# Kernel tuning notes

Measured on AMD Instinct MI355X. Metric: run time of the kernel, lower is better.

The kernel has to match this reference:

```python
import jax, jax.numpy as jnp
import numpy as np

B, N, D, S = 128, 1024, 512, 64
ITERS = 3
EPS = 1e-8


def setup_inputs() -> dict:
    key = jax.random.key(0)
    ks = jax.random.split(key, 10)
    inp = {
        "inputs_pe": jax.random.normal(ks[0], (B, N, D), dtype=jnp.float32),
        "inputs": jax.random.normal(ks[1], (B, N, D), dtype=jnp.float32),
        "slots": jax.random.normal(ks[2], (1, S, D), dtype=jnp.float32),
        "W1": jax.random.normal(ks[3], (D, D), dtype=jnp.float32) * 0.02,
        "b1": jnp.zeros((D,), dtype=jnp.float32),
        "W2": jax.random.normal(ks[4], (D, D), dtype=jnp.float32) * 0.02,
        "b2": jnp.zeros((D,), dtype=jnp.float32),
        "W3": jax.random.normal(ks[5], (D, D), dtype=jnp.float32) * 0.02,
        "b3": jnp.zeros((D,), dtype=jnp.float32),
    }
    return inp


def reference(inputs_pe, inputs, slots, W1, b1, W2, b2, W3, b3):
    b = inputs_pe.shape[0]
    scale = D ** (-0.5)
    # to_k: Linear -> ReLU -> Linear -> ReLU -> Linear (torch Linear: x @ W.T + b)
    h = jax.nn.relu(jnp.einsum('bnd,ed->bne', inputs_pe, W1) + b1)
    h = jax.nn.relu(jnp.einsum('bnd,ed->bne', h, W2) + b2)
    k = jnp.einsum('bnd,ed->bne', h, W3) + b3  # [b, n, d]

    q = jnp.broadcast_to(slots, (b, S, D))  # slots never updated in the loop
    for _ in range(ITERS):
        dots = jnp.einsum('bid,bjd->bij', q, k) * scale  # [b, S, n]
        s_j = dots.sum(axis=2, keepdims=True)            # sum over keys j -> [b, S, 1]
        s_all = dots.sum(axis=(1, 2), keepdims=True)     # total per batch -> [b, 1, 1]
        dots = dots / s_j * s_all
        attn = jax.nn.sigmoid(dots)
        attn2 = attn / (attn.sum(axis=-1, keepdims=True) + EPS)
        updates = jnp.einsum('bjd,bij->bid', inputs, attn2)  # [b, S, d]
    return updates, attn
```

## Files before the change

kernel.cpp:

```cpp
#include <hip/hip_runtime.h>
#include <stdint.h>

#define Bb 128
#define Nn 1024
#define Dd 512
#define Ss 64

constexpr float kScale = 0.044194173824159216f;
constexpr float kEps = 1e-8f;

typedef __bf16 bf16x8 __attribute__((ext_vector_type(8)));
typedef float f32x4 __attribute__((ext_vector_type(4)));
typedef float f32x16 __attribute__((ext_vector_type(16)));

#define MFMA32 __builtin_amdgcn_mfma_f32_32x32x16_bf16

__device__ inline unsigned short f2bf_rne(float x) {
  unsigned u = __builtin_bit_cast(unsigned, x);
  u += 0x7FFFu + ((u >> 16) & 1u);
  return (unsigned short)(u >> 16);
}
__device__ inline float bf2f(unsigned short h) {
  unsigned u = ((unsigned)h) << 16;
  return __builtin_bit_cast(float, u);
}

__device__ inline void gl_lds16(const void* g, void* l) {
  typedef unsigned int u32;
  auto gp = (u32 __attribute__((address_space(1)))*)(unsigned long long)(uintptr_t)g;
  auto lp = (u32 __attribute__((address_space(3)))*)(unsigned int)(uintptr_t)l;
  __builtin_amdgcn_global_load_lds(gp, lp, 16, 0, 0);
}

__global__ void cast_split(const float* __restrict__ in,
                           unsigned short* __restrict__ hi,
                           unsigned short* __restrict__ lo,
                           int n4) {
  int i = blockIdx.x * blockDim.x + threadIdx.x;
  const int stride = gridDim.x * blockDim.x;
  for (; i < n4; i += stride) {
    const float4 v = ((const float4*)in)[i];
    ushort4 h, lw;
    h.x = f2bf_rne(v.x); lw.x = f2bf_rne(v.x - bf2f(h.x));
    h.y = f2bf_rne(v.y); lw.y = f2bf_rne(v.y - bf2f(h.y));
    h.z = f2bf_rne(v.z); lw.z = f2bf_rne(v.z - bf2f(h.z));
    h.w = f2bf_rne(v.w); lw.w = f2bf_rne(v.w - bf2f(h.w));
    ((ushort4*)hi)[i] = h;
    ((ushort4*)lo)[i] = lw;
  }
}

template <int ACT>
__global__ __launch_bounds__(512, 1) void gemm_hp(
    const unsigned short* __restrict__ Ah, const unsigned short* __restrict__ Al,
    const unsigned short* __restrict__ Wh, const unsigned short* __restrict__ Wl,
    const float* __restrict__ bias,
    unsigned short* __restrict__ Ch, unsigned short* __restrict__ Cl) {
  constexpr int NH = 32;
  extern __shared__ unsigned short lds[];
  const int t = threadIdx.x, l = t & 63, w = t >> 6;
  const int wr = w >> 2, wc = w & 3;

  const int wg = ((blockIdx.x & 7) << 7) + (blockIdx.x >> 3);
  const long rowA0 = (long)(wg >> 1) * 256;
  const int colB0 = (wg & 1) * 256;

  const unsigned short* sbase =
      (w < 4) ? ((w < 2) ? Ah + rowA0 * 512 : Al + rowA0 * 512)
              : ((w < 6) ? Wh + (long)colB0 * 512 : Wl + (long)colB0 * 512);
  const int lcb = (w & 1) * 4;
  const int gsw = (l & 1) ^ ((l >> 3) & 1);
  const unsigned short* src0 = sbase + (lcb * 32 + (l >> 1)) * 512 + gsw * 8;
  const int dst0 = (w >> 1) * 4096 + lcb * 512;

#define STG(h)                                                            \
  {                                                                       \
    unsigned short* bq_ = lds + ((h) & 3) * 16384;                        \
    _Pragma("unroll") for (int j = 0; j < 4; j++)                         \
        gl_lds16(src0 + j * 16384 + (h) * 16, bq_ + dst0 + j * 512);      \
  }

  const int p8 = ((l >> 5) ^ ((l >> 2) & 1)) * 8;
  const int abase0 = (wr * 128 + (l & 31)) * 16 + p8;
  const int bbase0 = 8192 + (wc * 64 + (l & 31)) * 16 + p8;

#define READF(h, S)                                                       \
  {                                                                       \
    const unsigned short* bq_ = lds + ((h) & 3) * 16384;                  \
    _Pragma("unroll") for (int m = 0; m < 4; m++) {                       \
      ah##S[m] = *(const bf16x8*)(bq_ + abase0 + m * 512);                \
      al##S[m] = *(const bf16x8*)(bq_ + 4096 + abase0 + m * 512);         \
    }                                                                     \
    _Pragma("unroll") for (int n = 0; n < 2; n++) {                       \
      bh##S[n] = *(const bf16x8*)(bq_ + bbase0 + n * 512);                \
      bl##S[n] = *(const bf16x8*)(bq_ + 4096 + bbase0 + n * 512);         \
    }                                                                     \
  }

#define MFMACL(S)                                                         \
  {                                                                       \
    _Pragma("unroll") for (int m = 0; m < 4; m++)                         \
        _Pragma("unroll") for (int n = 0; n < 2; n++) {                   \
      acc[m][n] = MFMA32(ah##S[m], bh##S[n], acc[m][n], 0, 0, 0);         \
      acc[m][n] = MFMA32(al##S[m], bh##S[n], acc[m][n], 0, 0, 0);         \
      acc[m][n] = MFMA32(ah##S[m], bl##S[n], acc[m][n], 0, 0, 0);         \
    }                                                                     \
  }

#define BODY(h, CUR, NXT)                                                 \
  {                                                                       \
    asm volatile("s_waitcnt lgkmcnt(0)" ::: "memory");                    \
    __builtin_amdgcn_sched_barrier(0);                                    \
    if ((h) < 29) {                                                       \
      asm volatile("s_waitcnt vmcnt(8)" ::: "memory");                    \
    } else if ((h) == 29) {                                               \
      asm volatile("s_waitcnt vmcnt(4)" ::: "memory");                    \
    } else if ((h) == 30) {                                               \
      asm volatile("s_waitcnt vmcnt(0)" ::: "memory");                    \
    }                                                                     \
    __builtin_amdgcn_s_barrier();                                         \
    if ((h) + 4 < NH) STG((h) + 4);                                       \
    if ((h) + 1 < NH) READF((h) + 1, NXT);                                \
    __builtin_amdgcn_sched_barrier(0);                                    \
    __builtin_amdgcn_s_setprio(1);                                        \
    MFMACL(CUR);                                                          \
    __builtin_amdgcn_s_setprio(0);                                        \
  }

  f32x16 acc[4][2] = {};
  bf16x8 ahA[4], alA[4], bhA[2], blA[2];
  bf16x8 ahB[4], alB[4], bhB[2], blB[2];

  STG(0); STG(1); STG(2); STG(3);
  asm volatile("s_waitcnt vmcnt(12)" ::: "memory");
  __builtin_amdgcn_s_barrier();
  READF(0, A);

  for (int hh = 0; hh < NH; hh += 2) {
    BODY(hh, A, B);
    BODY(hh + 1, B, A);
  }
#undef STG
#undef READF
#undef MFMACL
#undef BODY

#pragma unroll
  for (int m = 0; m < 4; m++)
#pragma unroll
    for (int n = 0; n < 2; n++) {
      const int col = colB0 + wc * 64 + n * 32 + (l & 31);
      const float bv = bias[col];
#pragma unroll
      for (int r = 0; r < 16; r++) {
        const long row = rowA0 + wr * 128 + m * 32 + (r & 3) + 8 * (r >> 2) + 4 * (l >> 5);
        float xv = acc[m][n][r] + bv;
        if (ACT) xv = fmaxf(xv, 0.0f);
        const unsigned short h = f2bf_rne(xv);
        const long idx = row * 512 + col;
        Ch[idx] = h;
        Cl[idx] = f2bf_rne(xv - bf2f(h));
      }
    }
}

__global__ __launch_bounds__(256) void gemm_dots_split(
    const unsigned short* __restrict__ Qh, const unsigned short* __restrict__ Ql,
    const unsigned short* __restrict__ Kh, const unsigned short* __restrict__ Kl,
    float* __restrict__ dots) {
  constexpr int K = 512, BM = 64, BN = 128, BK = 32;
  __shared__ __align__(16) unsigned short lah[BM * BK];
  __shared__ __align__(16) unsigned short lal[BM * BK];
  __shared__ __align__(16) unsigned short lbh[BN * BK];
  __shared__ __align__(16) unsigned short lbl[BN * BK];
  const int t = threadIdx.x, l = t & 63, w = t >> 6;
  const int b = blockIdx.x >> 3, bc = blockIdx.x & 7;
  const unsigned short* kh = Kh + (long)b * Nn * Dd;
  const unsigned short* kl = Kl + (long)b * Nn * Dd;
  f32x4 acc[4][2] = {};

  for (int k0 = 0; k0 < K; k0 += BK) {
    {
      const int c = t;
      const int ga = (c >> 2) * K + k0 + (c & 3) * 8;
      const int lo = (w * 64) * 8;
      gl_lds16(Qh + ga, lah + lo);
      gl_lds16(Ql + ga, lal + lo);
    }
#pragma unroll
    for (int qq = 0; qq < 2; qq++) {
      const int c = qq * 256 + t;
      const long gb = (long)(bc * BN + (c >> 2)) * K + k0 + (c & 3) * 8;
      const int lo = (qq * 256 + w * 64) * 8;
      gl_lds16(kh + gb, lbh + lo);
      gl_lds16(kl + gb, lbl + lo);
    }
    __syncthreads();
    bf16x8 ah[4], al[4], bh[2], bl[2];
#pragma unroll
    for (int m = 0; m < 4; m++) {
      const int off = (m * 16 + (l & 15)) * BK + (l >> 4) * 8;
      ah[m] = *(const bf16x8*)(lah + off);
      al[m] = *(const bf16x8*)(lal + off);
    }
#pragma unroll
    for (int n = 0; n < 2; n++) {
      const int off = (w * 32 + n * 16 + (l & 15)) * BK + (l >> 4) * 8;
      bh[n] = *(const bf16x8*)(lbh + off);
      bl[n] = *(const bf16x8*)(lbl + off);
    }
#pragma unroll
    for (int m = 0; m < 4; m++)
#pragma unroll
      for (int n = 0; n < 2; n++) {
        acc[m][n] = __builtin_amdgcn_mfma_f32_16x16x32_bf16(ah[m], bh[n], acc[m][n], 0, 0, 0);
        acc[m][n] = __builtin_amdgcn_mfma_f32_16x16x32_bf16(al[m], bh[n], acc[m][n], 0, 0, 0);
        acc[m][n] = __builtin_amdgcn_mfma_f32_16x16x32_bf16(ah[m], bl[n], acc[m][n], 0, 0, 0);
      }
    __syncthreads();
  }
  float* dp = dots + (long)b * Ss * Nn;
#pragma unroll
  for (int m = 0; m < 4; m++) {
    const int row = m * 16 + (l >> 4) * 4;
#pragma unroll
    for (int n = 0; n < 2; n++) {
      const int col = bc * BN + w * 32 + n * 16 + (l & 15);
#pragma unroll
      for (int r = 0; r < 4; r++) dp[(long)(row + r) * Nn + col] = acc[m][n][r] * kScale;
    }
  }
}

__global__ __launch_bounds__(256) void reduce_k(
    const float* __restrict__ dots, float* __restrict__ s_j, float* __restrict__ s_all) {
  const int b = blockIdx.x;
  const int t = threadIdx.x;
  const float* dp = dots + (long)b * Ss * Nn;
  const int i = t >> 2, qq = t & 3;
  float s = 0.f;
  const float* rp = dp + i * Nn + qq * 256;
  for (int j = 0; j < 256; j++) s += rp[j];
  __shared__ float part[256];
  __shared__ float rowsum[64];
  part[t] = s;
  __syncthreads();
  if (t < 64) {
    const float v = part[t * 4] + part[t * 4 + 1] + part[t * 4 + 2] + part[t * 4 + 3];
    rowsum[t] = v;
    s_j[b * 64 + t] = v;
  }
  __syncthreads();
  if (t == 0) {
    float tot = 0.f;
    for (int k = 0; k < 64; k++) tot += rowsum[k];
    s_all[b] = tot;
  }
}

__global__ __launch_bounds__(256) void attn_k(
    const float* __restrict__ dots, const float* __restrict__ s_j,
    const float* __restrict__ s_all, float* __restrict__ attn_out,
    float* __restrict__ inv_r) {
  const int bi = blockIdx.x;
  const int b = bi >> 6;
  const int t = threadIdx.x;
  const float ratio = s_all[b] / s_j[bi];
  const float* dp = dots + (long)bi * Nn;
  float* ap = attn_out + (long)bi * Nn;
  float s = 0.f;
#pragma unroll
  for (int qq = 0; qq < 4; qq++) {
    const int j = qq * 256 + t;
    const float x = dp[j] * ratio;
    const float a = 1.f / (1.f + expf(-x));
    ap[j] = a;
    s += a;
  }
  __shared__ float red[256];
  red[t] = s;
  __syncthreads();
  for (int off = 128; off > 0; off >>= 1) {
    if (t < off) red[t] += red[t + off];
    __syncthreads();
  }
  if (t == 0) inv_r[bi] = 1.f / (red[0] + kEps);
}

__global__ __launch_bounds__(256, 1) void updates_k2(
    const float* __restrict__ attn, const float* __restrict__ inputs,
    const float* __restrict__ inv_r, float* __restrict__ out0) {
  constexpr int NT2 = 32;
  constexpr int BUF_F = 10240;
  extern __shared__ float ldsf[];
  const int t = threadIdx.x, lam = t & 63, w = t >> 6;
  const int b = blockIdx.x >> 1, dt = blockIdx.x & 1;
  const int ig = t >> 5, dg = t & 31;
  const float* inb = inputs + (size_t)b * (Nn * Dd) + dt * 256;
  const float* attsrc = attn + (size_t)b * (Ss * Nn) + (size_t)(t >> 2) * Nn + (t & 3) * 8;
  float acc[8][8] = {};
  float4 ga0, ga1, gb0, gb1;

#define UISSUE(bufi, tile, G0, G1)                                        \
  {                                                                       \
    const int j0_ = (tile)*32;                                            \
    G0 = *(const float4*)(attsrc + j0_);                                  \
    G1 = *(const float4*)(attsrc + j0_ + 4);                              \
    float* db_ = ldsf + (bufi)*BUF_F;                                     \
    _Pragma("unroll") for (int i_ = 0; i_ < 8; i_++) {                    \
      const int row_ = i_ * 4 + w;                                        \
      gl_lds16(inb + (size_t)(j0_ + row_) * Dd + lam * 4, db_ + row_ * 256); \
    }                                                                     \
  }

#define UWRITE(bufi, G0, G1)                                              \
  {                                                                       \
    float* ab_ = ldsf + (bufi)*BUF_F + 8192;                              \
    const int col_ = t >> 2;                                              \
    const int r0_ = (t & 3) * 8;                                          \
    ab_[(r0_ + 0) * 64 + col_] = G0.x;                                    \
    ab_[(r0_ + 1) * 64 + col_] = G0.y;                                    \
    ab_[(r0_ + 2) * 64 + col_] = G0.z;                                    \
    ab_[(r0_ + 3) * 64 + col_] = G0.w;                                    \
    ab_[(r0_ + 4) * 64 + col_] = G1.x;                                    \
    ab_[(r0_ + 5) * 64 + col_] = G1.y;                                    \
    ab_[(r0_ + 6) * 64 + col_] = G1.z;                                    \
    ab_[(r0_ + 7) * 64 + col_] = G1.w;                                    \
  }

#define UCOMP(bufi)                                                       \
  {                                                                       \
    const float* db_ = ldsf + (bufi)*BUF_F;                               \
    const float* ab_ = db_ + 8192;                                        \
    _Pragma("unroll 4") for (int jj = 0; jj < 32; jj++) {                 \
      float av[8], vv[8];                                                 \
      *(float4*)&av[0] = *(const float4*)(ab_ + jj * 64 + ig * 8);        \
      *(float4*)&av[4] = *(const float4*)(ab_ + jj * 64 + ig * 8 + 4);    \
      *(float4*)&vv[0] = *(const float4*)(db_ + jj * 256 + dg * 8);       \
      *(float4*)&vv[4] = *(const float4*)(db_ + jj * 256 + dg * 8 + 4);   \
      _Pragma("unroll") for (int m_ = 0; m_ < 8; m_++)                    \
          _Pragma("unroll") for (int n_ = 0; n_ < 8; n_++)                \
              acc[m_][n_] = __builtin_fmaf(av[m_], vv[n_], acc[m_][n_]);  \
    }                                                                     \
  }

  UISSUE(0, 0, ga0, ga1);
  UISSUE(1, 1, gb0, gb1);
  UWRITE(0, ga0, ga1);

  for (int tt = 0; tt < NT2; tt += 2) {
    asm volatile("s_waitcnt vmcnt(10)" ::: "memory");
    UWRITE((tt + 1) % 3, gb0, gb1);
    asm volatile("s_waitcnt lgkmcnt(0)" ::: "memory");
    __builtin_amdgcn_s_barrier();
    __builtin_amdgcn_sched_barrier(0);
    if (tt < NT2 - 2) UISSUE((tt + 2) % 3, tt + 2, ga0, ga1);
    UCOMP(tt % 3);
    if (tt + 1 < NT2 - 1) {
      asm volatile("s_waitcnt vmcnt(10)" ::: "memory");
    } else {
      asm volatile("s_waitcnt vmcnt(0)" ::: "memory");
    }
    if (tt + 1 < NT2 - 1) UWRITE((tt + 2) % 3, ga0, ga1);
    asm volatile("s_waitcnt lgkmcnt(0)" ::: "memory");
    __builtin_amdgcn_s_barrier();
    __builtin_amdgcn_sched_barrier(0);
    if (tt + 1 < NT2 - 2) UISSUE((tt + 3) % 3, tt + 3, gb0, gb1);
    UCOMP((tt + 1) % 3);
  }
#undef UISSUE
#undef UWRITE
#undef UCOMP

#pragma unroll
  for (int m = 0; m < 8; m++) {
    const int i = ig * 8 + m;
    const float ir = inv_r[b * 64 + i];
    float4 o0, o1;
    o0.x = acc[m][0] * ir; o0.y = acc[m][1] * ir; o0.z = acc[m][2] * ir; o0.w = acc[m][3] * ir;
    o1.x = acc[m][4] * ir; o1.y = acc[m][5] * ir; o1.z = acc[m][6] * ir; o1.w = acc[m][7] * ir;
    float* op = out0 + (size_t)(b * 64 + i) * Dd + dt * 256 + dg * 8;
    *(float4*)op = o0;
    *(float4*)(op + 4) = o1;
  }
}

extern "C" void kernel_launch(void* const* d_in, const int* in_sizes, int n_in,
                              void* d_out, int out_size, void* d_ws, size_t ws_size,
                              hipStream_t stream) {
  (void)in_sizes; (void)n_in; (void)out_size; (void)ws_size;
  const float* inputs_pe = (const float*)d_in[0];
  const float* inputs = (const float*)d_in[1];
  const float* slots = (const float*)d_in[2];
  const float* W1 = (const float*)d_in[3];
  const float* b1 = (const float*)d_in[4];
  const float* W2 = (const float*)d_in[5];
  const float* b2 = (const float*)d_in[6];
  const float* W3 = (const float*)d_in[7];
  const float* b3 = (const float*)d_in[8];

  char* ws = (char*)d_ws;
  size_t off = 0;
  auto alloc = [&](size_t bytes) -> void* {
    void* p = ws + off;
    off += (bytes + 255) & ~(size_t)255;
    return p;
  };
  const size_t actB = (size_t)Bb * Nn * Dd * 2;
  unsigned short* Ahi = (unsigned short*)alloc(actB);
  unsigned short* Alo = (unsigned short*)alloc(actB);
  unsigned short* Bhi = (unsigned short*)alloc(actB);
  unsigned short* Blo = (unsigned short*)alloc(actB);
  unsigned short* w1h = (unsigned short*)alloc(Dd * Dd * 2);
  unsigned short* w1l = (unsigned short*)alloc(Dd * Dd * 2);
  unsigned short* w2h = (unsigned short*)alloc(Dd * Dd * 2);
  unsigned short* w2l = (unsigned short*)alloc(Dd * Dd * 2);
  unsigned short* w3h = (unsigned short*)alloc(Dd * Dd * 2);
  unsigned short* w3l = (unsigned short*)alloc(Dd * Dd * 2);
  unsigned short* sh = (unsigned short*)alloc(Ss * Dd * 2);
  unsigned short* sl = (unsigned short*)alloc(Ss * Dd * 2);
  float* dotsb = (float*)alloc((size_t)Bb * Ss * Nn * 4);
  float* s_j = (float*)alloc(Bb * Ss * 4);
  float* s_all = (float*)alloc(Bb * 4);
  float* inv_r = (float*)alloc(Bb * Ss * 4);

  float* out_updates = (float*)d_out;
  float* out_attn = out_updates + (size_t)Bb * Ss * Dd;

  const int kLdsG = 4 * 32 * 1024;
  const int kLdsU = 3 * 40 * 1024;
  hipFuncSetAttribute(reinterpret_cast<const void*>(gemm_hp<1>),
                      hipFuncAttributeMaxDynamicSharedMemorySize, kLdsG);
  hipFuncSetAttribute(reinterpret_cast<const void*>(gemm_hp<0>),
                      hipFuncAttributeMaxDynamicSharedMemorySize, kLdsG);
  hipFuncSetAttribute(reinterpret_cast<const void*>(updates_k2),
                      hipFuncAttributeMaxDynamicSharedMemorySize, kLdsU);

  cast_split<<<4096, 256, 0, stream>>>(inputs_pe, Ahi, Alo, Bb * Nn * Dd / 4);
  cast_split<<<256, 256, 0, stream>>>(W1, w1h, w1l, Dd * Dd / 4);
  cast_split<<<256, 256, 0, stream>>>(W2, w2h, w2l, Dd * Dd / 4);
  cast_split<<<256, 256, 0, stream>>>(W3, w3h, w3l, Dd * Dd / 4);
  cast_split<<<32, 256, 0, stream>>>(slots, sh, sl, Ss * Dd / 4);

  gemm_hp<1><<<1024, 512, kLdsG, stream>>>(Ahi, Alo, w1h, w1l, b1, Bhi, Blo);
  gemm_hp<1><<<1024, 512, kLdsG, stream>>>(Bhi, Blo, w2h, w2l, b2, Ahi, Alo);
  gemm_hp<0><<<1024, 512, kLdsG, stream>>>(Ahi, Alo, w3h, w3l, b3, Bhi, Blo);

  gemm_dots_split<<<Bb * 8, 256, 0, stream>>>(sh, sl, Bhi, Blo, dotsb);
  reduce_k<<<Bb, 256, 0, stream>>>(dotsb, s_j, s_all);
  attn_k<<<Bb * Ss, 256, 0, stream>>>(dotsb, s_j, s_all, out_attn, inv_r);
  updates_k2<<<Bb * 2, 256, kLdsU, stream>>>(out_attn, inputs, inv_r, out_updates);
}
```

Before: 1.107 ms.

## Interleave bf16 hi/lo split planes into a single buffer for GEMM staging

```diff
diff --git a/kernel.cpp b/kernel.cpp
--- a/kernel.cpp
+++ b/kernel.cpp
@@ -12,6 +12,7 @@
 typedef __bf16 bf16x8 __attribute__((ext_vector_type(8)));
 typedef float f32x4 __attribute__((ext_vector_type(4)));
 typedef float f32x16 __attribute__((ext_vector_type(16)));
+typedef unsigned short ushort8 __attribute__((ext_vector_type(8)));
 
 #define MFMA32 __builtin_amdgcn_mfma_f32_32x32x16_bf16
 
@@ -32,30 +33,29 @@
   __builtin_amdgcn_global_load_lds(gp, lp, 16, 0, 0);
 }
 
-__global__ void cast_split(const float* __restrict__ in,
-                           unsigned short* __restrict__ hi,
-                           unsigned short* __restrict__ lo,
-                           int n4) {
+__global__ void cast_split_i(const float* __restrict__ in,
+                             unsigned short* __restrict__ out, int n8) {
   int i = blockIdx.x * blockDim.x + threadIdx.x;
   const int stride = gridDim.x * blockDim.x;
-  for (; i < n4; i += stride) {
-    const float4 v = ((const float4*)in)[i];
-    ushort4 h, lw;
-    h.x = f2bf_rne(v.x); lw.x = f2bf_rne(v.x - bf2f(h.x));
-    h.y = f2bf_rne(v.y); lw.y = f2bf_rne(v.y - bf2f(h.y));
-    h.z = f2bf_rne(v.z); lw.z = f2bf_rne(v.z - bf2f(h.z));
-    h.w = f2bf_rne(v.w); lw.w = f2bf_rne(v.w - bf2f(h.w));
-    ((ushort4*)hi)[i] = h;
-    ((ushort4*)lo)[i] = lw;
+  for (; i < n8; i += stride) {
+    const float4 v0 = ((const float4*)in)[i * 2];
+    const float4 v1 = ((const float4*)in)[i * 2 + 1];
+    float f[8] = {v0.x, v0.y, v0.z, v0.w, v1.x, v1.y, v1.z, v1.w};
+    ushort8 h, lo;
+#pragma unroll
+    for (int j = 0; j < 8; j++) {
+      h[j] = f2bf_rne(f[j]);
+      lo[j] = f2bf_rne(f[j] - bf2f(h[j]));
+    }
+    ((ushort8*)out)[i * 2] = h;
+    ((ushort8*)out)[i * 2 + 1] = lo;
   }
 }
 
 template <int ACT>
 __global__ __launch_bounds__(512, 1) void gemm_hp(
-    const unsigned short* __restrict__ Ah, const unsigned short* __restrict__ Al,
-    const unsigned short* __restrict__ Wh, const unsigned short* __restrict__ Wl,
-    const float* __restrict__ bias,
-    unsigned short* __restrict__ Ch, unsigned short* __restrict__ Cl) {
+    const unsigned short* __restrict__ A, const unsigned short* __restrict__ W,
+    const float* __restrict__ bias, unsigned short* __restrict__ C) {
   constexpr int NH = 32;
   extern __shared__ unsigned short lds[];
   const int t = threadIdx.x, l = t & 63, w = t >> 6;
@@ -65,35 +65,37 @@
   const long rowA0 = (long)(wg >> 1) * 256;
   const int colB0 = (wg & 1) * 256;
 
-  const unsigned short* sbase =
-      (w < 4) ? ((w < 2) ? Ah + rowA0 * 512 : Al + rowA0 * 512)
-              : ((w < 6) ? Wh + (long)colB0 * 512 : Wl + (long)colB0 * 512);
-  const int lcb = (w & 1) * 4;
-  const int gsw = (l & 1) ^ ((l >> 3) & 1);
-  const unsigned short* src0 = sbase + (lcb * 32 + (l >> 1)) * 512 + gsw * 8;
-  const int dst0 = (w >> 1) * 4096 + lcb * 512;
-
+  const unsigned short* base8 = (w < 4) ? A + rowA0 * 1024 : W + (long)colB0 * 1024;
+  const int p2s = ((l >> 1) ^ (l >> 4)) & 1;
+  const unsigned short* srcp[4];
+  int dstp[4];
+#pragma unroll
+  for (int j = 0; j < 4; j++) {
+    const int cid = (w & 3) * 4 + j;
+    srcp[j] = base8 + (long)(cid * 16 + (l >> 2)) * 1024 + p2s * 16 + (l & 1) * 8;
+    dstp[j] = (w * 4 + j) * 512;
+  }
 #define STG(h)                                                            \
   {                                                                       \
     unsigned short* bq_ = lds + ((h) & 3) * 16384;                        \
     _Pragma("unroll") for (int j = 0; j < 4; j++)                         \
-        gl_lds16(src0 + j * 16384 + (h) * 16, bq_ + dst0 + j * 512);      \
-  }
-
-  const int p8 = ((l >> 5) ^ ((l >> 2) & 1)) * 8;
-  const int abase0 = (wr * 128 + (l & 31)) * 16 + p8;
-  const int bbase0 = 8192 + (wc * 64 + (l & 31)) * 16 + p8;
+        gl_lds16(srcp[j] + (h) * 32, bq_ + dstp[j]);                      \
+  }
+
+  const int pp16 = (((l >> 5) ^ ((l >> 2) & 1))) * 16;
+  const int abase0 = (wr * 128 + (l & 31)) * 32 + pp16;
+  const int bbase0 = 8192 + (wc * 64 + (l & 31)) * 32 + pp16;
 
 #define READF(h, S)                                                       \
   {                                                                       \
     const unsigned short* bq_ = lds + ((h) & 3) * 16384;                  \
     _Pragma("unroll") for (int m = 0; m < 4; m++) {                       \
-      ah##S[m] = *(const bf16x8*)(bq_ + abase0 + m * 512);                \
-      al##S[m] = *(const bf16x8*)(bq_ + 4096 + abase0 + m * 512);         \
+      ah##S[m] = *(const bf16x8*)(bq_ + abase0 + m * 1024);               \
+      al##S[m] = *(const bf16x8*)(bq_ + abase0 + m * 1024 + 8);           \
     }                                                                     \
     _Pragma("unroll") for (int n = 0; n < 2; n++) {                       \
-      bh##S[n] = *(const bf16x8*)(bq_ + bbase0 + n * 512);                \
-      bl##S[n] = *(const bf16x8*)(bq_ + 4096 + bbase0 + n * 512);         \
+      bh##S[n] = *(const bf16x8*)(bq_ + bbase0 + n * 1024);               \
+      bl##S[n] = *(const bf16x8*)(bq_ + bbase0 + n * 1024 + 8);           \
     }                                                                     \
   }
 
@@ -151,22 +153,22 @@
     for (int n = 0; n < 2; n++) {
       const int col = colB0 + wc * 64 + n * 32 + (l & 31);
       const float bv = bias[col];
+      const int cofs = (col >> 3) * 16 + (col & 7);
 #pragma unroll
       for (int r = 0; r < 16; r++) {
         const long row = rowA0 + wr * 128 + m * 32 + (r & 3) + 8 * (r >> 2) + 4 * (l >> 5);
         float xv = acc[m][n][r] + bv;
         if (ACT) xv = fmaxf(xv, 0.0f);
         const unsigned short h = f2bf_rne(xv);
-        const long idx = row * 512 + col;
-        Ch[idx] = h;
-        Cl[idx] = f2bf_rne(xv - bf2f(h));
+        unsigned short* cp = C + row * 1024 + cofs;
+        cp[0] = h;
+        cp[8] = f2bf_rne(xv - bf2f(h));
       }
     }
 }
 
 __global__ __launch_bounds__(256) void gemm_dots_split(
-    const unsigned short* __restrict__ Qh, const unsigned short* __restrict__ Ql,
-    const unsigned short* __restrict__ Kh, const unsigned short* __restrict__ Kl,
+    const unsigned short* __restrict__ QI, const unsigned short* __restrict__ KI,
     float* __restrict__ dots) {
   constexpr int K = 512, BM = 64, BN = 128, BK = 32;
   __shared__ __align__(16) unsigned short lah[BM * BK];
@@ -175,26 +177,22 @@
   __shared__ __align__(16) unsigned short lbl[BN * BK];
   const int t = threadIdx.x, l = t & 63, w = t >> 6;
   const int b = blockIdx.x >> 3, bc = blockIdx.x & 7;
-  const unsigned short* kh = Kh + (long)b * Nn * Dd;
-  const unsigned short* kl = Kl + (long)b * Nn * Dd;
+  const unsigned short* kb = KI + (long)b * Nn * 1024;
   f32x4 acc[4][2] = {};
 
+  const int qbase = (t >> 2) * 1024 + (t & 3) * 16;
+  const long kbase0 = (long)(bc * BN + (t >> 2)) * 1024 + (t & 3) * 16;
+  const long kbase1 = (long)(bc * BN + 64 + (t >> 2)) * 1024 + (t & 3) * 16;
+
   for (int k0 = 0; k0 < K; k0 += BK) {
-    {
-      const int c = t;
-      const int ga = (c >> 2) * K + k0 + (c & 3) * 8;
-      const int lo = (w * 64) * 8;
-      gl_lds16(Qh + ga, lah + lo);
-      gl_lds16(Ql + ga, lal + lo);
-    }
-#pragma unroll
-    for (int qq = 0; qq < 2; qq++) {
-      const int c = qq * 256 + t;
-      const long gb = (long)(bc * BN + (c >> 2)) * K + k0 + (c & 3) * 8;
-      const int lo = (qq * 256 + w * 64) * 8;
-      gl_lds16(kh + gb, lbh + lo);
-      gl_lds16(kl + gb, lbl + lo);
-    }
+    const int ko = k0 * 2;
+    const int lo = w * 512;
+    gl_lds16(QI + qbase + ko, lah + lo);
+    gl_lds16(QI + qbase + ko + 8, lal + lo);
+    gl_lds16(kb + kbase0 + ko, lbh + lo);
+    gl_lds16(kb + kbase0 + ko + 8, lbl + lo);
+    gl_lds16(kb + kbase1 + ko, lbh + 2048 + lo);
+    gl_lds16(kb + kbase1 + ko + 8, lbl + 2048 + lo);
     __syncthreads();
     bf16x8 ah[4], al[4], bh[2], bl[2];
 #pragma unroll
@@ -406,19 +404,13 @@
     off += (bytes + 255) & ~(size_t)255;
     return p;
   };
-  const size_t actB = (size_t)Bb * Nn * Dd * 2;
-  unsigned short* Ahi = (unsigned short*)alloc(actB);
-  unsigned short* Alo = (unsigned short*)alloc(actB);
-  unsigned short* Bhi = (unsigned short*)alloc(actB);
-  unsigned short* Blo = (unsigned short*)alloc(actB);
-  unsigned short* w1h = (unsigned short*)alloc(Dd * Dd * 2);
-  unsigned short* w1l = (unsigned short*)alloc(Dd * Dd * 2);
-  unsigned short* w2h = (unsigned short*)alloc(Dd * Dd * 2);
-  unsigned short* w2l = (unsigned short*)alloc(Dd * Dd * 2);
-  unsigned short* w3h = (unsigned short*)alloc(Dd * Dd * 2);
-  unsigned short* w3l = (unsigned short*)alloc(Dd * Dd * 2);
-  unsigned short* sh = (unsigned short*)alloc(Ss * Dd * 2);
-  unsigned short* sl = (unsigned short*)alloc(Ss * Dd * 2);
+  const size_t actB = (size_t)Bb * Nn * 1024 * 2;
+  unsigned short* AI = (unsigned short*)alloc(actB);
+  unsigned short* BI = (unsigned short*)alloc(actB);
+  unsigned short* w1i = (unsigned short*)alloc(Dd * 1024 * 2);
+  unsigned short* w2i = (unsigned short*)alloc(Dd * 1024 * 2);
+  unsigned short* w3i = (unsigned short*)alloc(Dd * 1024 * 2);
+  unsigned short* qi = (unsigned short*)alloc(Ss * 1024 * 2);
   float* dotsb = (float*)alloc((size_t)Bb * Ss * Nn * 4);
   float* s_j = (float*)alloc(Bb * Ss * 4);
   float* s_all = (float*)alloc(Bb * 4);
@@ -436,17 +428,17 @@
   hipFuncSetAttribute(reinterpret_cast<const void*>(updates_k2),
                       hipFuncAttributeMaxDynamicSharedMemorySize, kLdsU);
 
-  cast_split<<<4096, 256, 0, stream>>>(inputs_pe, Ahi, Alo, Bb * Nn * Dd / 4);
-  cast_split<<<256, 256, 0, stream>>>(W1, w1h, w1l, Dd * Dd / 4);
-  cast_split<<<256, 256, 0, stream>>>(W2, w2h, w2l, Dd * Dd / 4);
-  cast_split<<<256, 256, 0, stream>>>(W3, w3h, w3l, Dd * Dd / 4);
-  cast_split<<<32, 256, 0, stream>>>(slots, sh, sl, Ss * Dd / 4);
-
-  gemm_hp<1><<<1024, 512, kLdsG, stream>>>(Ahi, Alo, w1h, w1l, b1, Bhi, Blo);
-  gemm_hp<1><<<1024, 512, kLdsG, stream>>>(Bhi, Blo, w2h, w2l, b2, Ahi, Alo);
-  gemm_hp<0><<<1024, 512, kLdsG, stream>>>(Ahi, Alo, w3h, w3l, b3, Bhi, Blo);
-
-  gemm_dots_split<<<Bb * 8, 256, 0, stream>>>(sh, sl, Bhi, Blo, dotsb);
+  cast_split_i<<<4096, 256, 0, stream>>>(inputs_pe, AI, Bb * Nn * Dd / 8);
+  cast_split_i<<<128, 256, 0, stream>>>(W1, w1i, Dd * Dd / 8);
+  cast_split_i<<<128, 256, 0, stream>>>(W2, w2i, Dd * Dd / 8);
+  cast_split_i<<<128, 256, 0, stream>>>(W3, w3i, Dd * Dd / 8);
+  cast_split_i<<<16, 256, 0, stream>>>(slots, qi, Ss * Dd / 8);
+
+  gemm_hp<1><<<1024, 512, kLdsG, stream>>>(AI, w1i, b1, BI);
+  gemm_hp<1><<<1024, 512, kLdsG, stream>>>(BI, w2i, b2, AI);
+  gemm_hp<0><<<1024, 512, kLdsG, stream>>>(AI, w3i, b3, BI);
+
+  gemm_dots_split<<<Bb * 8, 256, 0, stream>>>(qi, BI, dotsb);
   reduce_k<<<Bb, 256, 0, stream>>>(dotsb, s_j, s_all);
   attn_k<<<Bb * Ss, 256, 0, stream>>>(dotsb, s_j, s_all, out_attn, inv_r);
   updates_k2<<<Bb * 2, 256, kLdsU, stream>>>(out_attn, inputs, inv_r, out_updates);
```

Result: faster. 1.030 ms (-6.9%).
